# Kernel optimization log

Hardware: AMD Instinct MI355X
Metric: run time of the kernel (lower is better)

Reference implementation:

```python
import jax, jax.numpy as jnp
import numpy as np

SEQ, BATCH, D_IN, D_H = 512, 64, 1024, 1024


def setup_inputs() -> dict:
    key = jax.random.key(0)
    ks = jax.random.split(key, 5)
    scale_ih = 1.0 / np.sqrt(D_IN)
    scale_hh = 1.0 / np.sqrt(D_H)
    return {
        "x": jax.random.normal(ks[0], (SEQ, BATCH, D_IN), dtype=jnp.float32),
        "h0": jnp.zeros((BATCH, D_H), dtype=jnp.float32),
        "W_ih": jax.random.normal(ks[1], (D_H, D_IN), dtype=jnp.float32) * scale_ih,
        "b_ih": jax.random.normal(ks[2], (D_H,), dtype=jnp.float32) * scale_ih,
        "W_hh": jax.random.normal(ks[3], (D_H, D_H), dtype=jnp.float32) * scale_hh,
        "b_hh": jax.random.normal(ks[4], (D_H,), dtype=jnp.float32) * scale_hh,
    }


def reference(x, h0, W_ih, b_ih, W_hh, b_hh):
    # Elman RNN: h_t = tanh(x_t @ W_ih^T + b_ih + h_{t-1} @ W_hh^T + b_hh)
    # Input projection has no time dependency -> one big batched GEMM.
    x_proj = jnp.einsum("sbi,hi->sbh", x, W_ih) + b_ih + b_hh  # [S, B, H]

    def step(h_prev, xp_t):
        h_t = jnp.tanh(xp_t + h_prev @ W_hh.T)
        return h_t, h_t

    h_last, output = jax.lax.scan(step, h0, x_proj)
    return output, h_last  # ([S, B, H], [B, H])
```

## Files before the change

### kernel.cpp

```cpp
#include <hip/hip_runtime.h>
#include <hip/hip_cooperative_groups.h>
#include <cmath>

namespace cg = cooperative_groups;

#define SEQ   512
#define BATCH 64
#define DIN   1024
#define DH    1024

#define NREP   8
#define HS4    16657
#define HSF    (HS4 * 4)
#define PS4    (NREP * HS4)
#define PSF    (PS4 * 4)

typedef float f4 __attribute__((ext_vector_type(4)));

__global__ __launch_bounds__(256) void proj_kernel(
    const float* __restrict__ X, const float* __restrict__ W,
    const float* __restrict__ b_ih, const float* __restrict__ b_hh,
    float* __restrict__ C) {
  __shared__ float As[64][17];
  __shared__ float Bs[64][17];
  const int m0 = blockIdx.x * 64;
  const int n0 = blockIdx.y * 64;
  const int tid = threadIdx.x;
  const int tm = tid >> 4;
  const int tn = tid & 15;
  const int lrow = tid >> 2;
  const int lk4  = (tid & 3) * 4;

  float acc[4][4];
#pragma unroll
  for (int i = 0; i < 4; ++i)
#pragma unroll
    for (int j = 0; j < 4; ++j) acc[i][j] = 0.f;

  for (int kt = 0; kt < DIN; kt += 16) {
    float4 av = *(const float4*)(X + (size_t)(m0 + lrow) * DIN + kt + lk4);
    float4 bv = *(const float4*)(W + (size_t)(n0 + lrow) * DIN + kt + lk4);
    __syncthreads();
    As[lrow][lk4 + 0] = av.x; As[lrow][lk4 + 1] = av.y;
    As[lrow][lk4 + 2] = av.z; As[lrow][lk4 + 3] = av.w;
    Bs[lrow][lk4 + 0] = bv.x; Bs[lrow][lk4 + 1] = bv.y;
    Bs[lrow][lk4 + 2] = bv.z; Bs[lrow][lk4 + 3] = bv.w;
    __syncthreads();
#pragma unroll
    for (int kk = 0; kk < 16; ++kk) {
      float a[4], b[4];
#pragma unroll
      for (int i = 0; i < 4; ++i) a[i] = As[tm * 4 + i][kk];
#pragma unroll
      for (int j = 0; j < 4; ++j) b[j] = Bs[tn * 4 + j][kk];
#pragma unroll
      for (int i = 0; i < 4; ++i)
#pragma unroll
        for (int j = 0; j < 4; ++j) acc[i][j] += a[i] * b[j];
    }
  }

#pragma unroll
  for (int j = 0; j < 4; ++j) {
    const int n = n0 + tn * 4 + j;
    const float bias = b_ih[n] + b_hh[n];
#pragma unroll
    for (int i = 0; i < 4; ++i) {
      const int m = m0 + tm * 4 + i;
      C[(size_t)m * DH + n] = acc[i][j] + bias;
    }
  }
}

__global__ __launch_bounds__(256) void transpose_h0(
    const float* __restrict__ h0, float* __restrict__ hb, unsigned* cnt,
    int R) {
  const int idx = blockIdx.x * 256 + threadIdx.x;
  const int k4 = idx >> 6;
  const int b = idx & 63;
  float4 v = *(const float4*)(h0 + (size_t)b * DH + (k4 << 2));
  float4* h4 = (float4*)hb;
  for (int r = 0; r < R; ++r) h4[(size_t)r * HS4 + idx] = v;
  if (cnt != nullptr && blockIdx.x == 0 && threadIdx.x < 160) {
    __hip_atomic_store(&cnt[threadIdx.x], 0u, __ATOMIC_RELAXED,
                       __HIP_MEMORY_SCOPE_AGENT);
  }
}

__global__ __launch_bounds__(1024, 4) void rnn_fast(
    const float* __restrict__ W_hh, float* __restrict__ out,
    float* __restrict__ hb, unsigned* cnt) {
  __shared__ float red[4 * 1093];
  const int tid = threadIdx.x;
  const int bx = blockIdx.x;
  const int b = tid & 63;
  const int wv = tid >> 6;
  const int j0 = __builtin_amdgcn_readfirstlane(bx << 2);
  const float* __restrict__ w0 = W_hh + (size_t)j0 * DH;
  const float* __restrict__ w1 = w0 + DH;
  const float* __restrict__ w2 = w1 + DH;
  const float* __restrict__ w3 = w2 + DH;
  const int kq4 = __builtin_amdgcn_readfirstlane(wv << 4);
  const int fjj = tid & 3;
  const int fb  = tid >> 2;
  const int rep = __builtin_amdgcn_readfirstlane(bx & (NREP - 1));
  unsigned* leaf = cnt + ((bx & 7) << 4);
  unsigned* root = cnt + 128;
  unsigned* flag = cnt + 144;
  int sense = 1;
  bool dead = false;

  for (int t = 0; t < SEQ; ++t) {
    const f4* __restrict__ hp4 =
        (const f4*)hb + ((t & 1) ? PS4 : 0) + (size_t)rep * HS4;
    float* __restrict__ hn = hb + ((t & 1) ? 0 : PSF);
    const f4* pb = hp4 + (kq4 << 6) + b;

    f4 q0, q1, q2, q3, q4, q5, q6, q7, q8, q9, q10, q11, q12, q13, q14, q15;
#define LQ(i) asm volatile("global_load_dwordx4 %0, %1, off sc0 sc1" \
                           : "=v"(q##i) : "v"(pb + ((i) << 6)) : "memory");
    LQ(0)  LQ(1)  LQ(2)  LQ(3)  LQ(4)  LQ(5)  LQ(6)  LQ(7)
    LQ(8)  LQ(9)  LQ(10) LQ(11) LQ(12) LQ(13) LQ(14) LQ(15)
#undef LQ

    size_t ob = 0;
    float xp = 0.f;
    if (tid < 256) {
      ob = ((size_t)t * BATCH + fb) * DH + j0 + fjj;
      xp = out[ob];
    }

    asm volatile("s_waitcnt vmcnt(0)"
                 : "+v"(q0), "+v"(q1), "+v"(q2), "+v"(q3),
                   "+v"(q4), "+v"(q5), "+v"(q6), "+v"(q7),
                   "+v"(q8), "+v"(q9), "+v"(q10), "+v"(q11),
                   "+v"(q12), "+v"(q13), "+v"(q14), "+v"(q15)
                 :: "memory");

    float a0 = 0.f, a1 = 0.f, a2 = 0.f, a3 = 0.f;
#define CH(Q, c) { \
    const int k = (kq4 + (c)) << 2; \
    a0 = fmaf(w0[k + 0], Q.x, a0); a1 = fmaf(w1[k + 0], Q.x, a1); \
    a2 = fmaf(w2[k + 0], Q.x, a2); a3 = fmaf(w3[k + 0], Q.x, a3); \
    a0 = fmaf(w0[k + 1], Q.y, a0); a1 = fmaf(w1[k + 1], Q.y, a1); \
    a2 = fmaf(w2[k + 1], Q.y, a2); a3 = fmaf(w3[k + 1], Q.y, a3); \
    a0 = fmaf(w0[k + 2], Q.z, a0); a1 = fmaf(w1[k + 2], Q.z, a1); \
    a2 = fmaf(w2[k + 2], Q.z, a2); a3 = fmaf(w3[k + 2], Q.z, a3); \
    a0 = fmaf(w0[k + 3], Q.w, a0); a1 = fmaf(w1[k + 3], Q.w, a1); \
    a2 = fmaf(w2[k + 3], Q.w, a2); a3 = fmaf(w3[k + 3], Q.w, a3); \
  }
    CH(q0, 0)   CH(q1, 1)   CH(q2, 2)   CH(q3, 3)
    CH(q4, 4)   CH(q5, 5)   CH(q6, 6)   CH(q7, 7)
    CH(q8, 8)   CH(q9, 9)   CH(q10, 10) CH(q11, 11)
    CH(q12, 12) CH(q13, 13) CH(q14, 14) CH(q15, 15)
#undef CH

    red[0 * 1093 + b * 17 + wv] = a0;
    red[1 * 1093 + b * 17 + wv] = a1;
    red[2 * 1093 + b * 17 + wv] = a2;
    red[3 * 1093 + b * 17 + wv] = a3;
    __syncthreads();

    if (tid < 256) {
      float s = 0.f;
#pragma unroll
      for (int u = 0; u < 16; ++u) s += red[fjj * 1093 + fb * 17 + u];
      const float v = tanhf(xp + s);
      out[ob] = v;
      float* dst = hn + ((size_t)bx << 8) + tid;
#pragma unroll
      for (int r = 0; r < NREP; ++r) {
        asm volatile("global_store_dword %0, %1, off sc0 sc1"
                     :: "v"(dst + (size_t)r * HSF), "v"(v) : "memory");
      }
      if (t == SEQ - 1) {
        float* hl = out + (size_t)SEQ * BATCH * DH;
        hl[(size_t)fb * DH + j0 + fjj] = v;
      }
    }

    asm volatile("s_waitcnt vmcnt(0)" ::: "memory");
    __syncthreads();
    if (!dead && tid == 0) {
      unsigned old = __hip_atomic_fetch_add(leaf, 1u, __ATOMIC_RELAXED,
                                            __HIP_MEMORY_SCOPE_AGENT);
      if (old == 31u) {
        __hip_atomic_store(leaf, 0u, __ATOMIC_RELAXED,
                           __HIP_MEMORY_SCOPE_AGENT);
        asm volatile("s_waitcnt vmcnt(0)" ::: "memory");
        unsigned rold = __hip_atomic_fetch_add(root, 1u, __ATOMIC_RELAXED,
                                               __HIP_MEMORY_SCOPE_AGENT);
        if (rold == 7u) {
          __hip_atomic_store(root, 0u, __ATOMIC_RELAXED,
                             __HIP_MEMORY_SCOPE_AGENT);
          asm volatile("s_waitcnt vmcnt(0)" ::: "memory");
          __hip_atomic_store(flag, (unsigned)sense, __ATOMIC_RELAXED,
                             __HIP_MEMORY_SCOPE_AGENT);
        }
      }
      int guard = 0;
      while (__hip_atomic_load(flag, __ATOMIC_RELAXED,
                               __HIP_MEMORY_SCOPE_AGENT) != (unsigned)sense) {
        __builtin_amdgcn_s_sleep(1);
        if (++guard > (1 << 20)) { dead = true; break; }
      }
    }
    sense ^= 1;
    __syncthreads();
  }
}

__device__ __forceinline__ void rnn_step_body(
    float (*red)[4][64], const float4* __restrict__ hp,
    float* __restrict__ hn, const float* __restrict__ W_hh,
    float* __restrict__ out, int t, int bx, int tid) {
  const int b = tid & 63;
  const int wv = tid >> 6;
  const int j0 = __builtin_amdgcn_readfirstlane(bx << 2);
  const float* __restrict__ w0 = W_hh + (size_t)j0 * DH;
  const float* __restrict__ w1 = w0 + DH;
  const float* __restrict__ w2 = w1 + DH;
  const float* __restrict__ w3 = w2 + DH;
  const int kq4 = __builtin_amdgcn_readfirstlane(wv << 4);
  const int fjj = tid & 3;
  const int fb  = tid >> 2;

  const float4 q0  = hp[((kq4 +  0) << 6) + b];
  const float4 q1  = hp[((kq4 +  1) << 6) + b];
  const float4 q2  = hp[((kq4 +  2) << 6) + b];
  const float4 q3  = hp[((kq4 +  3) << 6) + b];
  const float4 q4  = hp[((kq4 +  4) << 6) + b];
  const float4 q5  = hp[((kq4 +  5) << 6) + b];
  const float4 q6  = hp[((kq4 +  6) << 6) + b];
  const float4 q7  = hp[((kq4 +  7) << 6) + b];
  const float4 q8  = hp[((kq4 +  8) << 6) + b];
  const float4 q9  = hp[((kq4 +  9) << 6) + b];
  const float4 q10 = hp[((kq4 + 10) << 6) + b];
  const float4 q11 = hp[((kq4 + 11) << 6) + b];
  const float4 q12 = hp[((kq4 + 12) << 6) + b];
  const float4 q13 = hp[((kq4 + 13) << 6) + b];
  const float4 q14 = hp[((kq4 + 14) << 6) + b];
  const float4 q15 = hp[((kq4 + 15) << 6) + b];

  size_t ob = 0;
  float xp = 0.f;
  if (tid < 256) {
    ob = ((size_t)t * BATCH + fb) * DH + j0 + fjj;
    xp = out[ob];
  }

  float a0 = 0.f, a1 = 0.f, a2 = 0.f, a3 = 0.f;
#define CH(Q, c) { \
    const int k = (kq4 + (c)) << 2; \
    a0 = fmaf(w0[k + 0], Q.x, a0); a1 = fmaf(w1[k + 0], Q.x, a1); \
    a2 = fmaf(w2[k + 0], Q.x, a2); a3 = fmaf(w3[k + 0], Q.x, a3); \
    a0 = fmaf(w0[k + 1], Q.y, a0); a1 = fmaf(w1[k + 1], Q.y, a1); \
    a2 = fmaf(w2[k + 1], Q.y, a2); a3 = fmaf(w3[k + 1], Q.y, a3); \
    a0 = fmaf(w0[k + 2], Q.z, a0); a1 = fmaf(w1[k + 2], Q.z, a1); \
    a2 = fmaf(w2[k + 2], Q.z, a2); a3 = fmaf(w3[k + 2], Q.z, a3); \
    a0 = fmaf(w0[k + 3], Q.w, a0); a1 = fmaf(w1[k + 3], Q.w, a1); \
    a2 = fmaf(w2[k + 3], Q.w, a2); a3 = fmaf(w3[k + 3], Q.w, a3); \
  }
  CH(q0, 0)   CH(q1, 1)   CH(q2, 2)   CH(q3, 3)
  CH(q4, 4)   CH(q5, 5)   CH(q6, 6)   CH(q7, 7)
  CH(q8, 8)   CH(q9, 9)   CH(q10, 10) CH(q11, 11)
  CH(q12, 12) CH(q13, 13) CH(q14, 14) CH(q15, 15)
#undef CH

  red[wv][0][b] = a0; red[wv][1][b] = a1;
  red[wv][2][b] = a2; red[wv][3][b] = a3;
  __syncthreads();

  if (tid < 256) {
    float s = 0.f;
#pragma unroll
    for (int u = 0; u < 16; ++u) s += red[u][fjj][fb];
    const float v = tanhf(xp + s);
    out[ob] = v;
    hn[((size_t)bx << 8) + tid] = v;
    if (t == SEQ - 1) {
      float* hl = out + (size_t)SEQ * BATCH * DH;
      hl[(size_t)fb * DH + j0 + fjj] = v;
    }
  }
}

__global__ __launch_bounds__(1024) void rnn_persistent_cg(
    const float* __restrict__ W_hh, float* __restrict__ out,
    float* __restrict__ hA, float* __restrict__ hB) {
  __shared__ float red[16][4][64];
  cg::grid_group grid = cg::this_grid();
  const int tid = threadIdx.x;
  const int bx = blockIdx.x;
  for (int t = 0; t < SEQ; ++t) {
    const float4* hp = (const float4*)((t & 1) ? hB : hA);
    float* hn = (t & 1) ? hA : hB;
    rnn_step_body(red, hp, hn, W_hh, out, t, bx, tid);
    grid.sync();
  }
}

__global__ __launch_bounds__(1024) void rnn_step_kernel(
    const float* __restrict__ hTprev, float* __restrict__ hTnext,
    const float* __restrict__ W_hh, float* __restrict__ out, int t) {
  __shared__ float red[16][4][64];
  rnn_step_body(red, (const float4*)hTprev, hTnext, W_hh, out, t,
                blockIdx.x, threadIdx.x);
}

extern "C" void kernel_launch(void* const* d_in, const int* in_sizes, int n_in,
                              void* d_out, int out_size, void* d_ws,
                              size_t ws_size, hipStream_t stream) {
  const float* x    = (const float*)d_in[0];
  const float* h0   = (const float*)d_in[1];
  const float* W_ih = (const float*)d_in[2];
  const float* b_ih = (const float*)d_in[3];
  const float* W_hh = (const float*)d_in[4];
  const float* b_hh = (const float*)d_in[5];
  float* out = (float*)d_out;
  unsigned* cnt = (unsigned*)d_ws;
  float* hb = (float*)d_ws + 256;
  const size_t need = 1024 + (size_t)2 * NREP * HSF * sizeof(float);
  const bool fast_ok = ws_size >= need;
  const bool fb_ok = ws_size >= 1024 + (size_t)2 * DH * BATCH * sizeof(float);

  hipLaunchKernelGGL(proj_kernel, dim3(512, 16), dim3(256), 0, stream,
                     x, W_ih, b_ih, b_hh, out);
  hipLaunchKernelGGL(transpose_h0, dim3(64), dim3(256), 0, stream, h0, hb,
                     fast_ok ? cnt : (unsigned*)nullptr, fast_ok ? NREP : 1);

  const float* W_hh_p = W_hh;
  float* out_p = out;
  float* hb_p = hb;
  float* hA_p = hb;
  float* hB_p = hb + (size_t)DH * BATCH;
  unsigned* cnt_p = cnt;
  hipError_t err = hipErrorUnknown;
  if (fast_ok) {
    void* args[] = {(void*)&W_hh_p, (void*)&out_p, (void*)&hb_p,
                    (void*)&cnt_p};
    err = hipLaunchCooperativeKernel(reinterpret_cast<void*>(rnn_fast),
                                     dim3(256), dim3(1024), args, 0, stream);
  }
  if (err != hipSuccess && fb_ok) {
    void* args2[] = {(void*)&W_hh_p, (void*)&out_p, (void*)&hA_p,
                     (void*)&hB_p};
    err = hipLaunchCooperativeKernel(
        reinterpret_cast<void*>(rnn_persistent_cg), dim3(256), dim3(1024),
        args2, 0, stream);
  }
  if (err != hipSuccess) {
    for (int t = 0; t < SEQ; ++t) {
      const float* src = (t & 1) ? hB_p : hA_p;
      float* dst = (t & 1) ? hA_p : hB_p;
      hipLaunchKernelGGL(rnn_step_kernel, dim3(256), dim3(1024), 0, stream,
                         src, dst, W_hh, out, t);
    }
  }
}
```

Before: 6.187 ms.

## Enlarge projection GEMM tiles and shrink recurrent grid to 64 blocks of 16 rows

The input-projection GEMM moves from 64x64 to 128x128 tiles with 8x8 register blocking, a transposed shared layout, and vectorised stores, to raise arithmetic intensity. The persistent recurrent kernel drops from 256 blocks with 4 hidden units each to 64 blocks with 16 hidden units each. The hidden-state replicas are removed, leaving a single copy per step. The barrier fan-in and load waits are adjusted to match. This cuts grid-barrier participants and replicated hidden-state stores, but leaves fewer CUs busy for the per-step matvec and makes each block stream four times as much of W_hh.

```diff
diff --git a/kernel.cpp b/kernel.cpp
--- a/kernel.cpp
+++ b/kernel.cpp
@@ -9,78 +9,88 @@
 #define DIN   1024
 #define DH    1024
 
-#define NREP   8
-#define HS4    16657
-#define HSF    (HS4 * 4)
-#define PS4    (NREP * HS4)
-#define PSF    (PS4 * 4)
+#define PSF 66624
+#define PS4 16656
 
 typedef float f4 __attribute__((ext_vector_type(4)));
 
-__global__ __launch_bounds__(256) void proj_kernel(
+__global__ __launch_bounds__(256, 4) void proj_kernel(
     const float* __restrict__ X, const float* __restrict__ W,
     const float* __restrict__ b_ih, const float* __restrict__ b_hh,
     float* __restrict__ C) {
-  __shared__ float As[64][17];
-  __shared__ float Bs[64][17];
-  const int m0 = blockIdx.x * 64;
-  const int n0 = blockIdx.y * 64;
+  __shared__ float As[16][132];
+  __shared__ float Bs[16][132];
+  const int m0 = blockIdx.x * 128;
+  const int n0 = blockIdx.y * 128;
   const int tid = threadIdx.x;
   const int tm = tid >> 4;
   const int tn = tid & 15;
   const int lrow = tid >> 2;
   const int lk4  = (tid & 3) * 4;
 
-  float acc[4][4];
-#pragma unroll
-  for (int i = 0; i < 4; ++i)
-#pragma unroll
-    for (int j = 0; j < 4; ++j) acc[i][j] = 0.f;
+  float acc[8][8];
+#pragma unroll
+  for (int i = 0; i < 8; ++i)
+#pragma unroll
+    for (int j = 0; j < 8; ++j) acc[i][j] = 0.f;
 
   for (int kt = 0; kt < DIN; kt += 16) {
-    float4 av = *(const float4*)(X + (size_t)(m0 + lrow) * DIN + kt + lk4);
-    float4 bv = *(const float4*)(W + (size_t)(n0 + lrow) * DIN + kt + lk4);
-    __syncthreads();
-    As[lrow][lk4 + 0] = av.x; As[lrow][lk4 + 1] = av.y;
-    As[lrow][lk4 + 2] = av.z; As[lrow][lk4 + 3] = av.w;
-    Bs[lrow][lk4 + 0] = bv.x; Bs[lrow][lk4 + 1] = bv.y;
-    Bs[lrow][lk4 + 2] = bv.z; Bs[lrow][lk4 + 3] = bv.w;
+    float4 av0 = *(const float4*)(X + (size_t)(m0 + lrow) * DIN + kt + lk4);
+    float4 av1 =
+        *(const float4*)(X + (size_t)(m0 + 64 + lrow) * DIN + kt + lk4);
+    float4 bv0 = *(const float4*)(W + (size_t)(n0 + lrow) * DIN + kt + lk4);
+    float4 bv1 =
+        *(const float4*)(W + (size_t)(n0 + 64 + lrow) * DIN + kt + lk4);
+    __syncthreads();
+    As[lk4 + 0][lrow] = av0.x; As[lk4 + 1][lrow] = av0.y;
+    As[lk4 + 2][lrow] = av0.z; As[lk4 + 3][lrow] = av0.w;
+    As[lk4 + 0][64 + lrow] = av1.x; As[lk4 + 1][64 + lrow] = av1.y;
+    As[lk4 + 2][64 + lrow] = av1.z; As[lk4 + 3][64 + lrow] = av1.w;
+    Bs[lk4 + 0][lrow] = bv0.x; Bs[lk4 + 1][lrow] = bv0.y;
+    Bs[lk4 + 2][lrow] = bv0.z; Bs[lk4 + 3][lrow] = bv0.w;
+    Bs[lk4 + 0][64 + lrow] = bv1.x; Bs[lk4 + 1][64 + lrow] = bv1.y;
+    Bs[lk4 + 2][64 + lrow] = bv1.z; Bs[lk4 + 3][64 + lrow] = bv1.w;
     __syncthreads();
 #pragma unroll
     for (int kk = 0; kk < 16; ++kk) {
-      float a[4], b[4];
-#pragma unroll
-      for (int i = 0; i < 4; ++i) a[i] = As[tm * 4 + i][kk];
-#pragma unroll
-      for (int j = 0; j < 4; ++j) b[j] = Bs[tn * 4 + j][kk];
-#pragma unroll
-      for (int i = 0; i < 4; ++i)
-#pragma unroll
-        for (int j = 0; j < 4; ++j) acc[i][j] += a[i] * b[j];
-    }
-  }
-
-#pragma unroll
-  for (int j = 0; j < 4; ++j) {
-    const int n = n0 + tn * 4 + j;
-    const float bias = b_ih[n] + b_hh[n];
-#pragma unroll
-    for (int i = 0; i < 4; ++i) {
-      const int m = m0 + tm * 4 + i;
-      C[(size_t)m * DH + n] = acc[i][j] + bias;
-    }
+      const float4 af0 = *(const float4*)&As[kk][tm * 8];
+      const float4 af1 = *(const float4*)&As[kk][tm * 8 + 4];
+      const float4 bf0 = *(const float4*)&Bs[kk][tn * 8];
+      const float4 bf1 = *(const float4*)&Bs[kk][tn * 8 + 4];
+      const float a[8] = {af0.x, af0.y, af0.z, af0.w,
+                          af1.x, af1.y, af1.z, af1.w};
+      const float b[8] = {bf0.x, bf0.y, bf0.z, bf0.w,
+                          bf1.x, bf1.y, bf1.z, bf1.w};
+#pragma unroll
+      for (int i = 0; i < 8; ++i)
+#pragma unroll
+        for (int j = 0; j < 8; ++j) acc[i][j] = fmaf(a[i], b[j], acc[i][j]);
+    }
+  }
+
+  const int nb = n0 + tn * 8;
+  float bias[8];
+#pragma unroll
+  for (int j = 0; j < 8; ++j) bias[j] = b_ih[nb + j] + b_hh[nb + j];
+#pragma unroll
+  for (int i = 0; i < 8; ++i) {
+    const size_t row = (size_t)(m0 + tm * 8 + i) * DH + nb;
+    float4 s0 = {acc[i][0] + bias[0], acc[i][1] + bias[1],
+                 acc[i][2] + bias[2], acc[i][3] + bias[3]};
+    float4 s1 = {acc[i][4] + bias[4], acc[i][5] + bias[5],
+                 acc[i][6] + bias[6], acc[i][7] + bias[7]};
+    *(float4*)(C + row) = s0;
+    *(float4*)(C + row + 4) = s1;
   }
 }
 
 __global__ __launch_bounds__(256) void transpose_h0(
-    const float* __restrict__ h0, float* __restrict__ hb, unsigned* cnt,
-    int R) {
+    const float* __restrict__ h0, float* __restrict__ hb, unsigned* cnt) {
   const int idx = blockIdx.x * 256 + threadIdx.x;
   const int k4 = idx >> 6;
   const int b = idx & 63;
   float4 v = *(const float4*)(h0 + (size_t)b * DH + (k4 << 2));
-  float4* h4 = (float4*)hb;
-  for (int r = 0; r < R; ++r) h4[(size_t)r * HS4 + idx] = v;
+  ((float4*)hb)[idx] = v;
   if (cnt != nullptr && blockIdx.x == 0 && threadIdx.x < 160) {
     __hip_atomic_store(&cnt[threadIdx.x], 0u, __ATOMIC_RELAXED,
                        __HIP_MEMORY_SCOPE_AGENT);
@@ -90,20 +100,14 @@
 __global__ __launch_bounds__(1024, 4) void rnn_fast(
     const float* __restrict__ W_hh, float* __restrict__ out,
     float* __restrict__ hb, unsigned* cnt) {
-  __shared__ float red[4 * 1093];
+  __shared__ float red[16 * 1024];
   const int tid = threadIdx.x;
   const int bx = blockIdx.x;
   const int b = tid & 63;
   const int wv = tid >> 6;
-  const int j0 = __builtin_amdgcn_readfirstlane(bx << 2);
-  const float* __restrict__ w0 = W_hh + (size_t)j0 * DH;
-  const float* __restrict__ w1 = w0 + DH;
-  const float* __restrict__ w2 = w1 + DH;
-  const float* __restrict__ w3 = w2 + DH;
+  const int j0 = __builtin_amdgcn_readfirstlane(bx << 4);
+  const float* __restrict__ w = W_hh + (size_t)j0 * DH;
   const int kq4 = __builtin_amdgcn_readfirstlane(wv << 4);
-  const int fjj = tid & 3;
-  const int fb  = tid >> 2;
-  const int rep = __builtin_amdgcn_readfirstlane(bx & (NREP - 1));
   unsigned* leaf = cnt + ((bx & 7) << 4);
   unsigned* root = cnt + 128;
   unsigned* flag = cnt + 144;
@@ -111,10 +115,12 @@
   bool dead = false;
 
   for (int t = 0; t < SEQ; ++t) {
-    const f4* __restrict__ hp4 =
-        (const f4*)hb + ((t & 1) ? PS4 : 0) + (size_t)rep * HS4;
+    const f4* __restrict__ hp4 = (const f4*)hb + ((t & 1) ? PS4 : 0);
     float* __restrict__ hn = hb + ((t & 1) ? 0 : PSF);
     const f4* pb = hp4 + (kq4 << 6) + b;
+
+    const size_t ob = ((size_t)t * BATCH + b) * DH + j0 + wv;
+    const float xp = out[ob];
 
     f4 q0, q1, q2, q3, q4, q5, q6, q7, q8, q9, q10, q11, q12, q13, q14, q15;
 #define LQ(i) asm volatile("global_load_dwordx4 %0, %1, off sc0 sc1" \
@@ -123,60 +129,62 @@
     LQ(8)  LQ(9)  LQ(10) LQ(11) LQ(12) LQ(13) LQ(14) LQ(15)
 #undef LQ
 
-    size_t ob = 0;
-    float xp = 0.f;
-    if (tid < 256) {
-      ob = ((size_t)t * BATCH + fb) * DH + j0 + fjj;
-      xp = out[ob];
-    }
+    float a0 = 0.f, a1 = 0.f, a2 = 0.f, a3 = 0.f;
+    float a4 = 0.f, a5 = 0.f, a6 = 0.f, a7 = 0.f;
+    float a8 = 0.f, a9 = 0.f, a10 = 0.f, a11 = 0.f;
+    float a12 = 0.f, a13 = 0.f, a14 = 0.f, a15 = 0.f;
+
+#define FMAJ(jj, Q, k) \
+    a##jj = fmaf(w[(jj) * DH + (k) + 0], Q.x, a##jj); \
+    a##jj = fmaf(w[(jj) * DH + (k) + 1], Q.y, a##jj); \
+    a##jj = fmaf(w[(jj) * DH + (k) + 2], Q.z, a##jj); \
+    a##jj = fmaf(w[(jj) * DH + (k) + 3], Q.w, a##jj);
+#define CH(Q, c) { \
+    const int k = (kq4 + (c)) << 2; \
+    FMAJ(0, Q, k)  FMAJ(1, Q, k)  FMAJ(2, Q, k)  FMAJ(3, Q, k) \
+    FMAJ(4, Q, k)  FMAJ(5, Q, k)  FMAJ(6, Q, k)  FMAJ(7, Q, k) \
+    FMAJ(8, Q, k)  FMAJ(9, Q, k)  FMAJ(10, Q, k) FMAJ(11, Q, k) \
+    FMAJ(12, Q, k) FMAJ(13, Q, k) FMAJ(14, Q, k) FMAJ(15, Q, k) \
+  }
+
+    asm volatile("s_waitcnt vmcnt(8)"
+                 : "+v"(q0), "+v"(q1), "+v"(q2), "+v"(q3),
+                   "+v"(q4), "+v"(q5), "+v"(q6), "+v"(q7)
+                 :: "memory");
+    CH(q0, 0) CH(q1, 1) CH(q2, 2) CH(q3, 3)
+    CH(q4, 4) CH(q5, 5) CH(q6, 6) CH(q7, 7)
 
     asm volatile("s_waitcnt vmcnt(0)"
-                 : "+v"(q0), "+v"(q1), "+v"(q2), "+v"(q3),
-                   "+v"(q4), "+v"(q5), "+v"(q6), "+v"(q7),
-                   "+v"(q8), "+v"(q9), "+v"(q10), "+v"(q11),
+                 : "+v"(q8), "+v"(q9), "+v"(q10), "+v"(q11),
                    "+v"(q12), "+v"(q13), "+v"(q14), "+v"(q15)
                  :: "memory");
-
-    float a0 = 0.f, a1 = 0.f, a2 = 0.f, a3 = 0.f;
-#define CH(Q, c) { \
-    const int k = (kq4 + (c)) << 2; \
-    a0 = fmaf(w0[k + 0], Q.x, a0); a1 = fmaf(w1[k + 0], Q.x, a1); \
-    a2 = fmaf(w2[k + 0], Q.x, a2); a3 = fmaf(w3[k + 0], Q.x, a3); \
-    a0 = fmaf(w0[k + 1], Q.y, a0); a1 = fmaf(w1[k + 1], Q.y, a1); \
-    a2 = fmaf(w2[k + 1], Q.y, a2); a3 = fmaf(w3[k + 1], Q.y, a3); \
-    a0 = fmaf(w0[k + 2], Q.z, a0); a1 = fmaf(w1[k + 2], Q.z, a1); \
-    a2 = fmaf(w2[k + 2], Q.z, a2); a3 = fmaf(w3[k + 2], Q.z, a3); \
-    a0 = fmaf(w0[k + 3], Q.w, a0); a1 = fmaf(w1[k + 3], Q.w, a1); \
-    a2 = fmaf(w2[k + 3], Q.w, a2); a3 = fmaf(w3[k + 3], Q.w, a3); \
-  }
-    CH(q0, 0)   CH(q1, 1)   CH(q2, 2)   CH(q3, 3)
-    CH(q4, 4)   CH(q5, 5)   CH(q6, 6)   CH(q7, 7)
     CH(q8, 8)   CH(q9, 9)   CH(q10, 10) CH(q11, 11)
     CH(q12, 12) CH(q13, 13) CH(q14, 14) CH(q15, 15)
 #undef CH
-
-    red[0 * 1093 + b * 17 + wv] = a0;
-    red[1 * 1093 + b * 17 + wv] = a1;
-    red[2 * 1093 + b * 17 + wv] = a2;
-    red[3 * 1093 + b * 17 + wv] = a3;
-    __syncthreads();
-
-    if (tid < 256) {
-      float s = 0.f;
-#pragma unroll
-      for (int u = 0; u < 16; ++u) s += red[fjj * 1093 + fb * 17 + u];
-      const float v = tanhf(xp + s);
-      out[ob] = v;
-      float* dst = hn + ((size_t)bx << 8) + tid;
-#pragma unroll
-      for (int r = 0; r < NREP; ++r) {
-        asm volatile("global_store_dword %0, %1, off sc0 sc1"
-                     :: "v"(dst + (size_t)r * HSF), "v"(v) : "memory");
-      }
-      if (t == SEQ - 1) {
-        float* hl = out + (size_t)SEQ * BATCH * DH;
-        hl[(size_t)fb * DH + j0 + fjj] = v;
-      }
+#undef FMAJ
+
+    red[wv * 1024 + 0 * 64 + b]  = a0;  red[wv * 1024 + 1 * 64 + b]  = a1;
+    red[wv * 1024 + 2 * 64 + b]  = a2;  red[wv * 1024 + 3 * 64 + b]  = a3;
+    red[wv * 1024 + 4 * 64 + b]  = a4;  red[wv * 1024 + 5 * 64 + b]  = a5;
+    red[wv * 1024 + 6 * 64 + b]  = a6;  red[wv * 1024 + 7 * 64 + b]  = a7;
+    red[wv * 1024 + 8 * 64 + b]  = a8;  red[wv * 1024 + 9 * 64 + b]  = a9;
+    red[wv * 1024 + 10 * 64 + b] = a10; red[wv * 1024 + 11 * 64 + b] = a11;
+    red[wv * 1024 + 12 * 64 + b] = a12; red[wv * 1024 + 13 * 64 + b] = a13;
+    red[wv * 1024 + 14 * 64 + b] = a14; red[wv * 1024 + 15 * 64 + b] = a15;
+    __syncthreads();
+
+    float s = 0.f;
+#pragma unroll
+    for (int u = 0; u < 16; ++u) s += red[u * 1024 + wv * 64 + b];
+    const float v = tanhf(xp + s);
+    out[ob] = v;
+    float* dst = hn + ((size_t)bx << 10) + ((wv >> 2) << 8) + (b << 2) +
+                 (wv & 3);
+    asm volatile("global_store_dword %0, %1, off sc0 sc1"
+                 :: "v"(dst), "v"(v) : "memory");
+    if (t == SEQ - 1) {
+      float* hl = out + (size_t)SEQ * BATCH * DH;
+      hl[(size_t)b * DH + j0 + wv] = v;
     }
 
     asm volatile("s_waitcnt vmcnt(0)" ::: "memory");
@@ -184,7 +192,7 @@
     if (!dead && tid == 0) {
       unsigned old = __hip_atomic_fetch_add(leaf, 1u, __ATOMIC_RELAXED,
                                             __HIP_MEMORY_SCOPE_AGENT);
-      if (old == 31u) {
+      if (old == 7u) {
         __hip_atomic_store(leaf, 0u, __ATOMIC_RELAXED,
                            __HIP_MEMORY_SCOPE_AGENT);
         asm volatile("s_waitcnt vmcnt(0)" ::: "memory");
@@ -320,29 +328,28 @@
   float* out = (float*)d_out;
   unsigned* cnt = (unsigned*)d_ws;
   float* hb = (float*)d_ws + 256;
-  const size_t need = 1024 + (size_t)2 * NREP * HSF * sizeof(float);
-  const bool fast_ok = ws_size >= need;
-  const bool fb_ok = ws_size >= 1024 + (size_t)2 * DH * BATCH * sizeof(float);
-
-  hipLaunchKernelGGL(proj_kernel, dim3(512, 16), dim3(256), 0, stream,
+  const size_t need = 1024 + (size_t)2 * PSF * sizeof(float);
+  const bool ok = ws_size >= need;
+
+  hipLaunchKernelGGL(proj_kernel, dim3(256, 8), dim3(256), 0, stream,
                      x, W_ih, b_ih, b_hh, out);
   hipLaunchKernelGGL(transpose_h0, dim3(64), dim3(256), 0, stream, h0, hb,
-                     fast_ok ? cnt : (unsigned*)nullptr, fast_ok ? NREP : 1);
+                     ok ? cnt : (unsigned*)nullptr);
 
   const float* W_hh_p = W_hh;
   float* out_p = out;
   float* hb_p = hb;
   float* hA_p = hb;
-  float* hB_p = hb + (size_t)DH * BATCH;
+  float* hB_p = hb + PSF;
   unsigned* cnt_p = cnt;
   hipError_t err = hipErrorUnknown;
-  if (fast_ok) {
+  if (ok) {
     void* args[] = {(void*)&W_hh_p, (void*)&out_p, (void*)&hb_p,
                     (void*)&cnt_p};
     err = hipLaunchCooperativeKernel(reinterpret_cast<void*>(rnn_fast),
-                                     dim3(256), dim3(1024), args, 0, stream);
-  }
-  if (err != hipSuccess && fb_ok) {
+                                     dim3(64), dim3(1024), args, 0, stream);
+  }
+  if (err != hipSuccess && ok) {
     void* args2[] = {(void*)&W_hh_p, (void*)&out_p, (void*)&hA_p,
                      (void*)&hB_p};
     err = hipLaunchCooperativeKernel(
```

Result: slower. 10.40 ms (+68.1%).
